# Optimization experiments

Measured on AMD Instinct MI355X. Metric: run time of the kernel, lower is better.

The kernel has to match this reference:

```python
import jax, jax.numpy as jnp
import numpy as np

N, DIM = 4096, 512


def _pairwise_dist(feat):
    # Euclidean distance matrix (N, N) without materializing (N, N, dim).
    sq = jnp.sum(feat * feat, axis=1)  # (N,)
    d2 = sq[:, None] + sq[None, :] - 2.0 * (feat @ feat.T)
    d2 = jnp.maximum(d2, 0.0)
    # safe sqrt: zero distance -> 0 (matches torch.norm subgradient behavior)
    pos = d2 > 0.0
    return jnp.where(pos, jnp.sqrt(jnp.where(pos, d2, 1.0)), 0.0)


def _u_centered(feat):
    # Unbiased (U-centered) distance matrix, diagonal zeroed.
    n = feat.shape[0]
    a = _pairwise_dist(feat)                       # (N, N)
    row = jnp.sum(a, axis=0, keepdims=True) / (n - 2)
    col = jnp.sum(a, axis=1, keepdims=True) / (n - 2)
    tot = jnp.sum(a) / ((n - 1) * (n - 2))
    A = a - row - col + tot
    return A * (1.0 - jnp.eye(n, dtype=A.dtype))   # fill_diagonal_(0)


def setup_inputs() -> dict:
    key = jax.random.key(0)
    ka, kb = jax.random.split(key)
    feat_a = jax.random.normal(ka, (N, DIM), dtype=jnp.float32)
    feat_b = jax.random.normal(kb, (N, DIM), dtype=jnp.float32)
    return {"feat_a": feat_a, "feat_b": feat_b}


def reference(feat_a, feat_b):
    n = feat_a.shape[0]
    vec_A = _u_centered(feat_a).reshape(-1)
    vec_B = _u_centered(feat_b).reshape(-1)
    denom = n * (n - 3)
    sq_dcov_ab = jnp.dot(vec_A, vec_B) / denom
    sq_dcov_aa = jnp.dot(vec_A, vec_A) / denom
    sq_dcov_bb = jnp.dot(vec_B, vec_B) / denom
    return sq_dcov_ab / jnp.maximum(jnp.sqrt(sq_dcov_aa * sq_dcov_bb), 1e-9)
```

## Files before the change

kernel.cpp:

```cpp
#include <hip/hip_runtime.h>
#include <hip/hip_fp16.h>
#include <math.h>

typedef float    f32x4 __attribute__((ext_vector_type(4)));
typedef _Float16 f16x8 __attribute__((ext_vector_type(8)));
typedef unsigned short u16x4 __attribute__((ext_vector_type(4)));

#define NPTS 4096
#define DIM  512
#define NTB  64
#define NTILES (NTB*(NTB+1)/2)

#define WS_U_A   0
#define WS_U_B   4096
#define WS_PAB   8192
#define WS_PAA   (8192 + NTILES)
#define WS_PBB   (8192 + 2*NTILES)
#define WS_SQA   (8192 + 3*NTILES)
#define WS_SQB   (WS_SQA + NPTS)
#define WS_ZERO_DOUBLES WS_SQA
#define WS_F16_BYTE_OFF 262144ull
#define HELEMS ((size_t)NPTS * DIM)

__device__ __forceinline__ void gload16h(const _Float16* g, _Float16* lds) {
  __builtin_amdgcn_global_load_lds(
      (const __attribute__((address_space(1))) void*)g,
      (__attribute__((address_space(3))) void*)lds, 16, 0, 0);
}

__device__ __forceinline__ void map_tile(int raw, int& bi, int& bj) {
  const int g = (raw & 7) * 260 + (raw >> 3);
  if (g < 288) {
    const int s = g / 36, r = g % 36;
    int rj = (int)((sqrtf(8.f * r + 1.f) - 1.f) * 0.5f);
    while ((rj + 1) * (rj + 2) / 2 <= r) ++rj;
    while (rj * (rj + 1) / 2 > r) --rj;
    const int ri = r - rj * (rj + 1) / 2;
    bi = s * 8 + ri; bj = s * 8 + rj;
  } else {
    const int e = g - 288;
    const int s = e / 64, r = e % 64;
    int SBJ = 1;
    while (SBJ * (SBJ + 1) / 2 <= s) ++SBJ;
    const int SBI = s - SBJ * (SBJ - 1) / 2;
    bi = SBI * 8 + (r >> 3); bj = SBJ * 8 + (r & 7);
  }
}

__global__ __launch_bounds__(256) void split_kernel(
    const float* __restrict__ fa, const float* __restrict__ fb,
    _Float16* __restrict__ ha0, _Float16* __restrict__ ha1,
    _Float16* __restrict__ hb0, _Float16* __restrict__ hb1,
    double* __restrict__ ws)
{
  const int wave = threadIdx.x >> 6, lane = threadIdx.x & 63;
  const int row = blockIdx.x * 4 + wave;
  const float* src = blockIdx.y ? fb : fa;
  _Float16* o0 = blockIdx.y ? hb0 : ha0;
  _Float16* o1 = blockIdx.y ? hb1 : ha1;
  double*  dst = blockIdx.y ? (ws + WS_SQB) : (ws + WS_SQA);

  {
    const f32x4* p = (const f32x4*)(src + (size_t)row * DIM);
    double s = 0.0;
#pragma unroll
    for (int c = 0; c < DIM / 4 / 64; ++c) {
      f32x4 v = p[lane + c * 64];
      s += (double)v[0]*v[0] + (double)v[1]*v[1] + (double)v[2]*v[2] + (double)v[3]*v[3];
    }
    for (int off = 32; off; off >>= 1) s += __shfl_down(s, off);
    if (lane == 0) dst[row] = s;
  }

  const int band = row >> 6, sub = (row >> 4) & 3, r16 = row & 15;
  const int c = lane >> 2, g = lane & 3;

  const f32x4* p = (const f32x4*)(src + (size_t)row * DIM + lane * 8);
  f32x4 v0 = p[0], v1 = p[1];

  f16x8 h0, h1;
#pragma unroll
  for (int u = 0; u < 4; ++u) {
    float x = v0[u];
    _Float16 h = (_Float16)x;
    h0[u] = h;
    h1[u] = (_Float16)((x - (float)h) * 2048.0f);
    float y = v1[u];
    _Float16 hh = (_Float16)y;
    h0[u + 4] = hh;
    h1[u + 4] = (_Float16)((y - (float)hh) * 2048.0f);
  }
  const size_t base = ((size_t)(band * 16 + c) * 4 + sub) * 512 + (size_t)r16 * 32;
  const int gp = (g ^ ((r16 >> 1) & 3)) * 8;
  *(f16x8*)(o0 + base + gp) = h0;
  *(f16x8*)(o1 + base + gp) = h1;
}

__global__ void __launch_bounds__(512, 4)
gram_kernel(const _Float16* __restrict__ HA0, const _Float16* __restrict__ HA1,
            const _Float16* __restrict__ HB0, const _Float16* __restrict__ HB1,
            double* __restrict__ ws)
{
  int bi, bj; map_tile(blockIdx.x, bi, bj);
  const int i0 = bi * 64, j0 = bj * 64;
  const bool diag = (bi == bj);

  __shared__ _Float16 smem[32768];
  __shared__ double wred[8][2];

  const int t = threadIdx.x, wave = t >> 6, lane = t & 63;
  const int mat = wave >> 2, q = wave & 3;
  const int cq = lane & 15, rq = lane >> 4;

  const _Float16* S0 = mat ? HB0 : HA0;
  const _Float16* S1 = mat ? HB1 : HA1;

  f32x4 accM[4], accC[4];
#pragma unroll
  for (int b = 0; b < 4; ++b) { accM[b] = (f32x4){0,0,0,0}; accC[b] = (f32x4){0,0,0,0}; }

#define STAGE(cc, buf) {                                                        \
    _Float16* W = smem + (buf) * 16384 + mat * 8192 + q * 512;                  \
    const size_t bI = ((size_t)(bi * 16 + (cc)) * 4 + q) * 512 + lane * 8;      \
    const size_t bJ = ((size_t)(bj * 16 + (cc)) * 4 + q) * 512 + lane * 8;      \
    gload16h(S0 + bI, W);                                                       \
    gload16h(S1 + bI, W + 2048);                                                \
    gload16h(S0 + bJ, W + 4096);                                                \
    gload16h(S1 + bJ, W + 6144);                                                \
  }

  STAGE(0, 0)
  __syncthreads();

  const int fo = cq * 32 + ((rq ^ ((cq >> 1) & 3)) << 3);

#pragma unroll 1
  for (int c = 0; c < 16; ++c) {
    if (c < 15) STAGE(c + 1, (c + 1) & 1)
    const _Float16* P = smem + (c & 1) * 16384 + mat * 8192;

    f16x8 A0 = *(const f16x8*)(P +        q * 512 + fo);
    f16x8 A1 = *(const f16x8*)(P + 2048 + q * 512 + fo);
    f16x8 B0[4], B1[4];
#pragma unroll
    for (int tj = 0; tj < 4; ++tj) {
      B0[tj] = *(const f16x8*)(P + 4096 + tj * 512 + fo);
      B1[tj] = *(const f16x8*)(P + 6144 + tj * 512 + fo);
    }
#pragma unroll
    for (int tj = 0; tj < 4; ++tj) {
      accM[tj] = __builtin_amdgcn_mfma_f32_16x16x32_f16(A0, B0[tj], accM[tj], 0, 0, 0);
      accC[tj] = __builtin_amdgcn_mfma_f32_16x16x32_f16(A0, B1[tj], accC[tj], 0, 0, 0);
      accC[tj] = __builtin_amdgcn_mfma_f32_16x16x32_f16(A1, B0[tj], accC[tj], 0, 0, 0);
    }
    __syncthreads();
  }

  unsigned short* db = (unsigned short*)smem;

  const double* sqx = ws + (mat ? WS_SQB : WS_SQA);
  double*       uxp = ws + (mat ? WS_U_B : WS_U_A);

  double si[4], sj[4];
#pragma unroll
  for (int r = 0; r < 4; ++r) si[r] = sqx[i0 + q * 16 + rq * 4 + r];
#pragma unroll
  for (int tj = 0; tj < 4; ++tj) sj[tj] = sqx[j0 + tj * 16 + cq];

  double rs[4] = {0,0,0,0}, cs[4] = {0,0,0,0}, self = 0.0;
  unsigned short pk[4][4];

#pragma unroll
  for (int tj = 0; tj < 4; ++tj)
#pragma unroll
    for (int r = 0; r < 4; ++r) {
      double G = (double)accM[tj][r] + (double)accC[tj][r] * (1.0 / 2048.0);
      double d2 = si[r] + sj[tj] - 2.0 * G;
      unsigned short bits = 0;
      double dq = 0.0;
      if (d2 > 0.0) {
        float df = (float)sqrt(d2);
        __half h = __float2half(df);
        bits = __half_as_ushort(h);
        dq = (double)__half2float(h);
      }
      if (diag && (q * 16 + rq * 4 + r == tj * 16 + cq)) { bits = 0; dq = 0.0; }
      pk[tj][r] = bits;
      rs[r] += dq;
      cs[tj] += dq;
      self += dq * dq;
    }

  if (mat == 1) {
#pragma unroll
    for (int tj = 0; tj < 4; ++tj) {
      u16x4 v = {pk[tj][0], pk[tj][1], pk[tj][2], pk[tj][3]};
      *(u16x4*)(db + q * 1024 + lane * 16 + tj * 4) = v;
    }
  }

#pragma unroll
  for (int z = 0; z < 4; ++z) {
    double v = rs[z];
    v += __shfl_xor(v, 1); v += __shfl_xor(v, 2); v += __shfl_xor(v, 4); v += __shfl_xor(v, 8);
    if (cq == 0) atomicAdd(&uxp[i0 + q * 16 + rq * 4 + z], v);
  }
  if (!diag) {
#pragma unroll
    for (int tj = 0; tj < 4; ++tj) {
      double v = cs[tj];
      v += __shfl_xor(v, 16); v += __shfl_xor(v, 32);
      if (lane < 16) atomicAdd(&uxp[j0 + tj * 16 + cq], v);
    }
  }

  __syncthreads();

  double pab = 0.0;
  if (mat == 0) {
#pragma unroll
    for (int tj = 0; tj < 4; ++tj) {
      u16x4 vb = *(const u16x4*)(db + q * 1024 + lane * 16 + tj * 4);
#pragma unroll
      for (int r = 0; r < 4; ++r)
        pab += (double)__half2float(__ushort_as_half(pk[tj][r]))
             * (double)__half2float(__ushort_as_half(vb[r]));
    }
  }

  for (int off = 32; off; off >>= 1) {
    pab  += __shfl_down(pab, off);
    self += __shfl_down(self, off);
  }
  if (lane == 0) {
    wred[wave][0] = (mat == 0) ? pab  : self;
    wred[wave][1] = (mat == 0) ? self : 0.0;
  }
  __syncthreads();
  if (t == 0) {
    double w = diag ? 1.0 : 2.0;
    double s0 = 0, s1 = 0, s2 = 0;
    for (int z = 0; z < 4; ++z) { s0 += wred[z][0]; s1 += wred[z][1]; s2 += wred[4 + z][0]; }
    ws[WS_PAB + blockIdx.x] = w * s0;
    ws[WS_PAA + blockIdx.x] = w * s1;
    ws[WS_PBB + blockIdx.x] = w * s2;
  }
}

__global__ __launch_bounds__(256) void final_kernel(const double* __restrict__ ws,
                                                    float* __restrict__ out)
{
  const int t = threadIdx.x;
  double sa = 0, sb = 0, uab = 0, uaa = 0, ubb = 0, ab = 0, aa = 0, bb = 0;
  for (int i = t; i < NPTS; i += 256) {
    double a = ws[WS_U_A + i], b = ws[WS_U_B + i];
    sa += a; sb += b; uab += a * b; uaa += a * a; ubb += b * b;
  }
  for (int i = t; i < NTILES; i += 256) {
    ab += ws[WS_PAB + i]; aa += ws[WS_PAA + i]; bb += ws[WS_PBB + i];
  }
  for (int off = 32; off; off >>= 1) {
    sa  += __shfl_down(sa, off);  sb  += __shfl_down(sb, off);
    uab += __shfl_down(uab, off); uaa += __shfl_down(uaa, off); ubb += __shfl_down(ubb, off);
    ab  += __shfl_down(ab, off);  aa  += __shfl_down(aa, off);  bb  += __shfl_down(bb, off);
  }
  __shared__ double red[4][8];
  int wave = t >> 6, lane = t & 63;
  if (lane == 0) {
    red[wave][0] = sa;  red[wave][1] = sb;  red[wave][2] = uab; red[wave][3] = uaa;
    red[wave][4] = ubb; red[wave][5] = ab;  red[wave][6] = aa;  red[wave][7] = bb;
  }
  __syncthreads();
  if (t == 0) {
    double v[8] = {0,0,0,0,0,0,0,0};
    for (int qq = 0; qq < 4; ++qq) for (int z = 0; z < 8; ++z) v[z] += red[qq][z];
    const double SA = v[0], SB = v[1], UAB = v[2], UAA = v[3], UBB = v[4];
    const double PAB = v[5], PAA = v[6], PBB = v[7];
    const double n = (double)NPTS, nm2 = n - 2.0;
    auto dotv = [&](double P, double U, double sx, double sy) {
      double tX = sx / ((n - 1.0) * nm2), tY = sy / ((n - 1.0) * nm2);
      double RX = sx / nm2, RY = sy / nm2;
      double su  = U / nm2;
      double srr = U / (nm2 * nm2);
      double full = P - 4.0 * su + tY * sx + tX * sy + 2.0 * n * srr + 2.0 * RX * RY
                  - 2.0 * n * tY * RX - 2.0 * n * tX * RY + n * n * tX * tY;
      double dg = n * tX * tY - 2.0 * tX * RY - 2.0 * tY * RX + 4.0 * srr;
      return full - dg;
    };
    const double denomc = n * (n - 3.0);
    double dab = dotv(PAB, UAB, SA, SB) / denomc;
    double daa = dotv(PAA, UAA, SA, SA) / denomc;
    double dbb = dotv(PBB, UBB, SB, SB) / denomc;
    double dn = sqrt(daa * dbb);
    if (dn < 1e-9) dn = 1e-9;
    out[0] = (float)(dab / dn);
  }
}

extern "C" void kernel_launch(void* const* d_in, const int* in_sizes, int n_in,
                              void* d_out, int out_size, void* d_ws, size_t ws_size,
                              hipStream_t stream) {
  const float* fa = (const float*)d_in[0];
  const float* fb = (const float*)d_in[1];
  double* ws = (double*)d_ws;

  _Float16* HA0 = (_Float16*)((char*)d_ws + WS_F16_BYTE_OFF);
  _Float16* HA1 = HA0 + HELEMS;
  _Float16* HB0 = HA1 + HELEMS;
  _Float16* HB1 = HB0 + HELEMS;

  hipMemsetAsync(d_ws, 0, WS_ZERO_DOUBLES * sizeof(double), stream);
  split_kernel<<<dim3(NPTS / 4, 2), 256, 0, stream>>>(fa, fb, HA0, HA1, HB0, HB1, ws);
  gram_kernel<<<NTILES, 512, 0, stream>>>(HA0, HA1, HB0, HB1, ws);
  final_kernel<<<1, 256, 0, stream>>>(ws, (float*)d_out);
}
```

Measured before the change: 138.1 us.

## Load Gram operands directly from global into registers, halve waves per block

```diff
diff --git a/kernel.cpp b/kernel.cpp
--- a/kernel.cpp
+++ b/kernel.cpp
@@ -21,12 +21,6 @@
 #define WS_ZERO_DOUBLES WS_SQA
 #define WS_F16_BYTE_OFF 262144ull
 #define HELEMS ((size_t)NPTS * DIM)
-
-__device__ __forceinline__ void gload16h(const _Float16* g, _Float16* lds) {
-  __builtin_amdgcn_global_load_lds(
-      (const __attribute__((address_space(1))) void*)g,
-      (__attribute__((address_space(3))) void*)lds, 16, 0, 0);
-}
 
 __device__ __forceinline__ void map_tile(int raw, int& bi, int& bj) {
   const int g = (raw & 7) * 260 + (raw >> 3);
@@ -96,7 +90,7 @@
   *(f16x8*)(o1 + base + gp) = h1;
 }
 
-__global__ void __launch_bounds__(512, 4)
+__global__ void __launch_bounds__(256, 3)
 gram_kernel(const _Float16* __restrict__ HA0, const _Float16* __restrict__ HA1,
             const _Float16* __restrict__ HB0, const _Float16* __restrict__ HB1,
             double* __restrict__ ws)
@@ -105,105 +99,104 @@
   const int i0 = bi * 64, j0 = bj * 64;
   const bool diag = (bi == bj);
 
-  __shared__ _Float16 smem[32768];
-  __shared__ double wred[8][2];
+  __shared__ unsigned short db[2][64][32];
+  __shared__ double wred[4][2];
 
   const int t = threadIdx.x, wave = t >> 6, lane = t & 63;
-  const int mat = wave >> 2, q = wave & 3;
+  const int mat = wave >> 1, h = wave & 1;
   const int cq = lane & 15, rq = lane >> 4;
 
   const _Float16* S0 = mat ? HB0 : HA0;
   const _Float16* S1 = mat ? HB1 : HA1;
 
-  f32x4 accM[4], accC[4];
-#pragma unroll
-  for (int b = 0; b < 4; ++b) { accM[b] = (f32x4){0,0,0,0}; accC[b] = (f32x4){0,0,0,0}; }
-
-#define STAGE(cc, buf) {                                                        \
-    _Float16* W = smem + (buf) * 16384 + mat * 8192 + q * 512;                  \
-    const size_t bI = ((size_t)(bi * 16 + (cc)) * 4 + q) * 512 + lane * 8;      \
-    const size_t bJ = ((size_t)(bj * 16 + (cc)) * 4 + q) * 512 + lane * 8;      \
-    gload16h(S0 + bI, W);                                                       \
-    gload16h(S1 + bI, W + 2048);                                                \
-    gload16h(S0 + bJ, W + 4096);                                                \
-    gload16h(S1 + bJ, W + 6144);                                                \
-  }
-
-  STAGE(0, 0)
-  __syncthreads();
-
-  const int fo = cq * 32 + ((rq ^ ((cq >> 1) & 3)) << 3);
+  const int laneoff = cq * 32 + ((rq ^ ((cq >> 1) & 3)) << 3);
+
+  const _Float16* pA0 = S0 + ((size_t)(bi * 16) * 4 + h * 2) * 512 + laneoff;
+  const _Float16* pA1 = S1 + ((size_t)(bi * 16) * 4 + h * 2) * 512 + laneoff;
+  const _Float16* pB0 = S0 + ((size_t)(bj * 16) * 4) * 512 + laneoff;
+  const _Float16* pB1 = S1 + ((size_t)(bj * 16) * 4) * 512 + laneoff;
+
+  f32x4 accM[2][4], accC[2][4];
+#pragma unroll
+  for (int a = 0; a < 2; ++a)
+#pragma unroll
+    for (int b = 0; b < 4; ++b) { accM[a][b] = (f32x4){0,0,0,0}; accC[a][b] = (f32x4){0,0,0,0}; }
 
 #pragma unroll 1
   for (int c = 0; c < 16; ++c) {
-    if (c < 15) STAGE(c + 1, (c + 1) & 1)
-    const _Float16* P = smem + (c & 1) * 16384 + mat * 8192;
-
-    f16x8 A0 = *(const f16x8*)(P +        q * 512 + fo);
-    f16x8 A1 = *(const f16x8*)(P + 2048 + q * 512 + fo);
-    f16x8 B0[4], B1[4];
+    f16x8 A0[2], A1[2];
+#pragma unroll
+    for (int ti = 0; ti < 2; ++ti) {
+      A0[ti] = *(const f16x8*)(pA0 + ti * 512);
+      A1[ti] = *(const f16x8*)(pA1 + ti * 512);
+    }
 #pragma unroll
     for (int tj = 0; tj < 4; ++tj) {
-      B0[tj] = *(const f16x8*)(P + 4096 + tj * 512 + fo);
-      B1[tj] = *(const f16x8*)(P + 6144 + tj * 512 + fo);
+      f16x8 B0 = *(const f16x8*)(pB0 + tj * 512);
+      f16x8 B1 = *(const f16x8*)(pB1 + tj * 512);
+#pragma unroll
+      for (int ti = 0; ti < 2; ++ti) {
+        accM[ti][tj] = __builtin_amdgcn_mfma_f32_16x16x32_f16(A0[ti], B0, accM[ti][tj], 0, 0, 0);
+        accC[ti][tj] = __builtin_amdgcn_mfma_f32_16x16x32_f16(A0[ti], B1, accC[ti][tj], 0, 0, 0);
+        accC[ti][tj] = __builtin_amdgcn_mfma_f32_16x16x32_f16(A1[ti], B0, accC[ti][tj], 0, 0, 0);
+      }
     }
-#pragma unroll
-    for (int tj = 0; tj < 4; ++tj) {
-      accM[tj] = __builtin_amdgcn_mfma_f32_16x16x32_f16(A0, B0[tj], accM[tj], 0, 0, 0);
-      accC[tj] = __builtin_amdgcn_mfma_f32_16x16x32_f16(A0, B1[tj], accC[tj], 0, 0, 0);
-      accC[tj] = __builtin_amdgcn_mfma_f32_16x16x32_f16(A1, B0[tj], accC[tj], 0, 0, 0);
-    }
-    __syncthreads();
-  }
-
-  unsigned short* db = (unsigned short*)smem;
+    pA0 += 2048; pA1 += 2048; pB0 += 2048; pB1 += 2048;
+  }
 
   const double* sqx = ws + (mat ? WS_SQB : WS_SQA);
   double*       uxp = ws + (mat ? WS_U_B : WS_U_A);
 
-  double si[4], sj[4];
-#pragma unroll
-  for (int r = 0; r < 4; ++r) si[r] = sqx[i0 + q * 16 + rq * 4 + r];
+  double si[8], sj[4];
+#pragma unroll
+  for (int ti = 0; ti < 2; ++ti)
+#pragma unroll
+    for (int r = 0; r < 4; ++r)
+      si[ti * 4 + r] = sqx[i0 + h * 32 + ti * 16 + rq * 4 + r];
 #pragma unroll
   for (int tj = 0; tj < 4; ++tj) sj[tj] = sqx[j0 + tj * 16 + cq];
 
-  double rs[4] = {0,0,0,0}, cs[4] = {0,0,0,0}, self = 0.0;
-  unsigned short pk[4][4];
-
-#pragma unroll
-  for (int tj = 0; tj < 4; ++tj)
-#pragma unroll
-    for (int r = 0; r < 4; ++r) {
-      double G = (double)accM[tj][r] + (double)accC[tj][r] * (1.0 / 2048.0);
-      double d2 = si[r] + sj[tj] - 2.0 * G;
-      unsigned short bits = 0;
-      double dq = 0.0;
-      if (d2 > 0.0) {
-        float df = (float)sqrt(d2);
-        __half h = __float2half(df);
-        bits = __half_as_ushort(h);
-        dq = (double)__half2float(h);
+  double rs[8] = {0,0,0,0,0,0,0,0}, cs[4] = {0,0,0,0}, self = 0.0;
+  unsigned short pk[2][4][4];
+
+#pragma unroll
+  for (int ti = 0; ti < 2; ++ti)
+#pragma unroll
+    for (int tj = 0; tj < 4; ++tj)
+#pragma unroll
+      for (int r = 0; r < 4; ++r) {
+        double G = (double)accM[ti][tj][r] + (double)accC[ti][tj][r] * (1.0 / 2048.0);
+        double d2 = si[ti * 4 + r] + sj[tj] - 2.0 * G;
+        unsigned short bits = 0;
+        double dq = 0.0;
+        if (d2 > 0.0) {
+          float df = (float)sqrt(d2);
+          __half hh = __float2half(df);
+          bits = __half_as_ushort(hh);
+          dq = (double)__half2float(hh);
+        }
+        if (diag && (h * 32 + ti * 16 + rq * 4 + r == tj * 16 + cq)) { bits = 0; dq = 0.0; }
+        pk[ti][tj][r] = bits;
+        rs[ti * 4 + r] += dq;
+        cs[tj] += dq;
+        self += dq * dq;
       }
-      if (diag && (q * 16 + rq * 4 + r == tj * 16 + cq)) { bits = 0; dq = 0.0; }
-      pk[tj][r] = bits;
-      rs[r] += dq;
-      cs[tj] += dq;
-      self += dq * dq;
-    }
 
   if (mat == 1) {
 #pragma unroll
-    for (int tj = 0; tj < 4; ++tj) {
-      u16x4 v = {pk[tj][0], pk[tj][1], pk[tj][2], pk[tj][3]};
-      *(u16x4*)(db + q * 1024 + lane * 16 + tj * 4) = v;
-    }
-  }
-
-#pragma unroll
-  for (int z = 0; z < 4; ++z) {
+    for (int ti = 0; ti < 2; ++ti)
+#pragma unroll
+      for (int tj = 0; tj < 4; ++tj) {
+        u16x4 v = {pk[ti][tj][0], pk[ti][tj][1], pk[ti][tj][2], pk[ti][tj][3]};
+        *(u16x4*)(&db[h][lane][(ti * 4 + tj) * 4]) = v;
+      }
+  }
+
+#pragma unroll
+  for (int z = 0; z < 8; ++z) {
     double v = rs[z];
     v += __shfl_xor(v, 1); v += __shfl_xor(v, 2); v += __shfl_xor(v, 4); v += __shfl_xor(v, 8);
-    if (cq == 0) atomicAdd(&uxp[i0 + q * 16 + rq * 4 + z], v);
+    if (cq == 0) atomicAdd(&uxp[i0 + h * 32 + (z >> 2) * 16 + rq * 4 + (z & 3)], v);
   }
   if (!diag) {
 #pragma unroll
@@ -219,13 +212,15 @@
   double pab = 0.0;
   if (mat == 0) {
 #pragma unroll
-    for (int tj = 0; tj < 4; ++tj) {
-      u16x4 vb = *(const u16x4*)(db + q * 1024 + lane * 16 + tj * 4);
-#pragma unroll
-      for (int r = 0; r < 4; ++r)
-        pab += (double)__half2float(__ushort_as_half(pk[tj][r]))
-             * (double)__half2float(__ushort_as_half(vb[r]));
-    }
+    for (int ti = 0; ti < 2; ++ti)
+#pragma unroll
+      for (int tj = 0; tj < 4; ++tj) {
+        u16x4 vb = *(const u16x4*)(&db[h][lane][(ti * 4 + tj) * 4]);
+#pragma unroll
+        for (int r = 0; r < 4; ++r)
+          pab += (double)__half2float(__ushort_as_half(pk[ti][tj][r]))
+               * (double)__half2float(__ushort_as_half(vb[r]));
+      }
   }
 
   for (int off = 32; off; off >>= 1) {
@@ -239,11 +234,9 @@
   __syncthreads();
   if (t == 0) {
     double w = diag ? 1.0 : 2.0;
-    double s0 = 0, s1 = 0, s2 = 0;
-    for (int z = 0; z < 4; ++z) { s0 += wred[z][0]; s1 += wred[z][1]; s2 += wred[4 + z][0]; }
-    ws[WS_PAB + blockIdx.x] = w * s0;
-    ws[WS_PAA + blockIdx.x] = w * s1;
-    ws[WS_PBB + blockIdx.x] = w * s2;
+    ws[WS_PAB + blockIdx.x] = w * (wred[0][0] + wred[1][0]);
+    ws[WS_PAA + blockIdx.x] = w * (wred[0][1] + wred[1][1]);
+    ws[WS_PBB + blockIdx.x] = w * (wred[2][0] + wred[3][0]);
   }
 }
 
@@ -311,6 +304,6 @@
 
   hipMemsetAsync(d_ws, 0, WS_ZERO_DOUBLES * sizeof(double), stream);
   split_kernel<<<dim3(NPTS / 4, 2), 256, 0, stream>>>(fa, fb, HA0, HA1, HB0, HB1, ws);
-  gram_kernel<<<NTILES, 512, 0, stream>>>(HA0, HA1, HB0, HB1, ws);
+  gram_kernel<<<NTILES, 256, 0, stream>>>(HA0, HA1, HB0, HB1, ws);
   final_kernel<<<1, 256, 0, stream>>>(ws, (float*)d_out);
 }
```

New measurement: 125.5 us. 1.1x faster.
